# Kernel optimization log

Hardware: AMD Instinct MI355X
Metric: run time of the kernel (lower is better)

The kernel has to match this reference:

```python
import jax, jax.numpy as jnp
import numpy as np

D_MODEL = 2048
N_HEADS = 16
D_HEAD = D_MODEL // N_HEADS
D_FF = 8192
EPS = 1e-6
ROPE_BASE = 10000.0


def rmsnorm(x, g):
    return x * jax.lax.rsqrt(jnp.mean(x * x, axis=-1, keepdims=True) + EPS) * g


def rotate_half(x):
    x1, x2 = jnp.split(x, 2, axis=-1)
    return jnp.concatenate((-x2, x1), axis=-1)


def rope_tables(T):
    inv_freq = 1.0 / (ROPE_BASE ** (jnp.arange(0, D_HEAD, 2, dtype=jnp.float32) / D_HEAD))
    freqs = jnp.arange(T, dtype=jnp.float32)[:, None] * inv_freq[None, :]  # [T, D_HEAD//2]
    emb = jnp.concatenate((freqs, freqs), axis=-1)  # [T, D_HEAD]
    return jnp.cos(emb), jnp.sin(emb)


def setup_inputs() -> dict:
    key = jax.random.key(0)
    ks = jax.random.split(key, 6)
    std = 0.02
    x = jax.random.normal(ks[0], (2, 2048, D_MODEL), dtype=jnp.float32)
    # weights stored (in, out) so forward is x @ W
    w_qkv = jax.random.normal(ks[1], (D_MODEL, 3 * D_MODEL), dtype=jnp.float32) * std
    w_out = jax.random.normal(ks[2], (D_MODEL, D_MODEL), dtype=jnp.float32) * std
    w_g = jax.random.normal(ks[3], (D_MODEL, D_FF), dtype=jnp.float32) * std
    w_u = jax.random.normal(ks[4], (D_MODEL, D_FF), dtype=jnp.float32) * std
    w_o = jax.random.normal(ks[5], (D_FF, D_MODEL), dtype=jnp.float32) * std
    g1 = jnp.ones((D_MODEL,), dtype=jnp.float32)
    g2 = jnp.ones((D_MODEL,), dtype=jnp.float32)
    return {"x": x, "w_qkv": w_qkv, "w_out": w_out, "g1": g1, "g2": g2,
            "w_g": w_g, "w_u": w_u, "w_o": w_o}


def reference(x, w_qkv, w_out, g1, g2, w_g, w_u, w_o):
    B, T, D = x.shape
    H, dh = N_HEADS, D_HEAD
    scale = dh ** -0.5

    h = rmsnorm(x, g1)
    qkv = h @ w_qkv  # [B, T, 3D]
    q, k, v = jnp.split(qkv, 3, axis=-1)
    # [B, H, T, dh]
    q = q.reshape(B, T, H, dh).transpose(0, 2, 1, 3)
    k = k.reshape(B, T, H, dh).transpose(0, 2, 1, 3)
    v = v.reshape(B, T, H, dh).transpose(0, 2, 1, 3)

    cos, sin = rope_tables(T)  # [T, dh] each
    cos = cos[None, None]
    sin = sin[None, None]
    q = q * cos + rotate_half(q) * sin
    k = k * cos + rotate_half(k) * sin

    scores = jnp.einsum('bhqd,bhkd->bhqk', q, k) * scale
    causal = jnp.arange(T)[None, :] <= jnp.arange(T)[:, None]  # [T, T]
    scores = jnp.where(causal[None, None], scores, -jnp.inf)
    attn = jax.nn.softmax(scores, axis=-1)
    ctx = jnp.einsum('bhqk,bhkd->bhqd', attn, v)  # [B, H, T, dh]
    ctx = ctx.transpose(0, 2, 1, 3).reshape(B, T, D)
    x = x + ctx @ w_out

    h = rmsnorm(x, g2)
    x = x + (jax.nn.silu(h @ w_g) * (h @ w_u)) @ w_o
    return x
```

## Files before the change

### kernel.cpp

```cpp
#include <hip/hip_runtime.h>

typedef __bf16 bf16x8 __attribute__((ext_vector_type(8)));
typedef float f32x4 __attribute__((ext_vector_type(4)));
typedef unsigned short u16x8 __attribute__((ext_vector_type(8)));

#define B_SZ 2
#define T_SEQ 2048
#define D_MODEL 2048
#define N_HEADS 16
#define D_HEAD 128
#define D_FF 8192
#define BT (B_SZ * T_SEQ)
#define NT (T_SEQ / 64)

__device__ __forceinline__ unsigned short f2bf(float f) {
  unsigned int u = __builtin_bit_cast(unsigned int, f);
  u += 0x7FFFu + ((u >> 16) & 1u);
  return (unsigned short)(u >> 16);
}
__device__ __forceinline__ float bf2f(unsigned short h) {
  unsigned int u = ((unsigned int)h) << 16;
  return __builtin_bit_cast(float, u);
}

__device__ __forceinline__ void load_lds16(const void* g, void* l) {
  __builtin_amdgcn_global_load_lds(
      (const __attribute__((address_space(1))) unsigned int*)g,
      (__attribute__((address_space(3))) unsigned int*)l, 16, 0, 0);
}

template <int N>
__device__ __forceinline__ void vm_gate() {
  if constexpr (N <= 0)
    asm volatile("s_waitcnt vmcnt(0)" ::: "memory");
  else if constexpr (N == 2)
    asm volatile("s_waitcnt vmcnt(2)" ::: "memory");
  else if constexpr (N == 3)
    asm volatile("s_waitcnt vmcnt(3)" ::: "memory");
  else if constexpr (N == 4)
    asm volatile("s_waitcnt vmcnt(4)" ::: "memory");
  else if constexpr (N == 6)
    asm volatile("s_waitcnt vmcnt(6)" ::: "memory");
  else
    asm volatile("s_waitcnt vmcnt(8)" ::: "memory");
}

__global__ __launch_bounds__(256) void transpose_cast_kernel(
    const float* __restrict__ in, unsigned short* __restrict__ out, int R, int C) {
  __shared__ float tile[64][65];
  const int tx = threadIdx.x, ty = threadIdx.y;
  const int c0 = blockIdx.x * 64, r0 = blockIdx.y * 64;
#pragma unroll
  for (int i = 0; i < 4; ++i) {
    const float4 v = *(const float4*)(in + (long)(r0 + ty + 16 * i) * C + c0 + tx * 4);
    float* tr = &tile[ty + 16 * i][tx * 4];
    tr[0] = v.x; tr[1] = v.y; tr[2] = v.z; tr[3] = v.w;
  }
  __syncthreads();
#pragma unroll
  for (int i = 0; i < 4; ++i) {
    const int cc = ty + 16 * i;
    ushort4 o;
    o.x = f2bf(tile[tx * 4 + 0][cc]);
    o.y = f2bf(tile[tx * 4 + 1][cc]);
    o.z = f2bf(tile[tx * 4 + 2][cc]);
    o.w = f2bf(tile[tx * 4 + 3][cc]);
    *(ushort4*)(out + (long)(c0 + cc) * R + r0 + tx * 4) = o;
  }
}

__global__ __launch_bounds__(256) void rmsnorm_cast_kernel(
    const float* __restrict__ x, const float* __restrict__ gw,
    unsigned short* __restrict__ out) {
  const int row = blockIdx.x;
  const int tid = threadIdx.x;
  const float* xr = x + (long)row * D_MODEL;
  float4 a = *(const float4*)(xr + tid * 8);
  float4 b = *(const float4*)(xr + tid * 8 + 4);
  float ss = a.x * a.x + a.y * a.y + a.z * a.z + a.w * a.w +
             b.x * b.x + b.y * b.y + b.z * b.z + b.w * b.w;
#pragma unroll
  for (int d = 1; d < 64; d <<= 1) ss += __shfl_xor(ss, d);
  __shared__ float part[4];
  if ((tid & 63) == 0) part[tid >> 6] = ss;
  __syncthreads();
  ss = part[0] + part[1] + part[2] + part[3];
  const float rs = rsqrtf(ss * (1.0f / D_MODEL) + 1e-6f);
  float4 g0 = *(const float4*)(gw + tid * 8);
  float4 g1 = *(const float4*)(gw + tid * 8 + 4);
  ushort4 o0, o1;
  o0.x = f2bf(a.x * rs * g0.x); o0.y = f2bf(a.y * rs * g0.y);
  o0.z = f2bf(a.z * rs * g0.z); o0.w = f2bf(a.w * rs * g0.w);
  o1.x = f2bf(b.x * rs * g1.x); o1.y = f2bf(b.y * rs * g1.y);
  o1.z = f2bf(b.z * rs * g1.z); o1.w = f2bf(b.w * rs * g1.w);
  unsigned short* op = out + (long)row * D_MODEL + tid * 8;
  *(ushort4*)op = o0;
  *(ushort4*)(op + 4) = o1;
}

template <int EPI, int WM, int WN, int FM, int FN, bool DUALA = false>
__global__ __launch_bounds__(WM * WN * 64, 2) void gemm_ks_kernel(
    const unsigned short* __restrict__ A, const unsigned short* __restrict__ Bt,
    void* __restrict__ Cout, const void* __restrict__ aux,
    const unsigned short* __restrict__ A2,
    int M, int N, int K, int lda, int ldb, int ldc, int cm, int cn) {
  constexpr int THREADS = WM * WN * 64;
  constexpr int BM = WM * FM * 16;
  constexpr int BN = WN * FN * 16;
  constexpr int ASLOT = BM * 32;
  constexpr int BSLOT = BN * 32;
  constexpr int RPR = THREADS / 4;
  constexpr int LPS = BM / RPR + BN / RPR;
  __shared__ unsigned short As[4 * ASLOT];
  __shared__ unsigned short Bs[4 * BSLOT];

  const int tid = threadIdx.x;
  const int lane = tid & 63, g = lane >> 4, c = lane & 15;
  const int w = tid >> 6, wr = w / WN, wc = w % WN;

  const int nbn = N / BN;
  const int bid = (int)blockIdx.x;
  const int xcd = bid & 7, idx = bid >> 3;
  const int chn = nbn / cn;
  const int crow = xcd / chn, ccol = xcd % chn;
  const int mr = idx / cn, nc2 = idx % cn;
  const int m0 = (crow * cm + mr) * BM;
  const int n0 = (ccol * cn + nc2) * BN;

  const int nks = K >> 5;
  const int srow = tid >> 2;
  const int kq8 = (tid & 3) * 8;
  const unsigned short* A_ = A + (long)m0 * lda;
  const unsigned short* A2_ = DUALA ? (A2 + (long)m0 * lda) : nullptr;
  const unsigned short* B_ = Bt + (long)n0 * ldb;

  auto stage = [&](int s) {
    const int slot = s & 3;
    const long k32 = (long)s * 32;
    const unsigned short* Ab;
    long akofs;
    if constexpr (DUALA) {
      const int khalf = K >> 1;
      const bool lo = k32 < khalf;
      Ab = lo ? A_ : A2_;
      akofs = (lo ? k32 : k32 - khalf) + kq8;
    } else {
      Ab = A_;
      akofs = k32 + kq8;
    }
    const long bkofs = k32 + kq8;
#pragma unroll
    for (int j = 0; j < BM / RPR; ++j)
      load_lds16(Ab + (long)(j * RPR + srow) * lda + akofs,
                 &As[slot * ASLOT + (j * THREADS + tid) * 8]);
#pragma unroll
    for (int j = 0; j < BN / RPR; ++j)
      load_lds16(B_ + (long)(j * RPR + srow) * ldb + bkofs,
                 &Bs[slot * BSLOT + (j * THREADS + tid) * 8]);
  };

  f32x4 acc[FM][FN] = {};

  stage(0);
  if (nks > 1) stage(1);
  if (nks > 2) stage(2);
  vm_gate<2 * LPS>();
  __builtin_amdgcn_sched_barrier(0);
  __builtin_amdgcn_s_barrier();

  for (int s = 0; s < nks; ++s) {
    const int slot = s & 3;
    const unsigned short* Ap = &As[slot * ASLOT] + (wr * FM * 16 + c) * 32 + g * 8;
    const unsigned short* Bp = &Bs[slot * BSLOT] + (wc * FN * 16 + c) * 32 + g * 8;
    bf16x8 fa[FM], fb[FN];
#pragma unroll
    for (int fm = 0; fm < FM; ++fm) fa[fm] = *(const bf16x8*)(Ap + fm * 512);
#pragma unroll
    for (int fn = 0; fn < FN; ++fn) fb[fn] = *(const bf16x8*)(Bp + fn * 512);
    if (s + 3 < nks) stage(s + 3);
    __builtin_amdgcn_s_setprio(1);
#pragma unroll
    for (int fm = 0; fm < FM; ++fm)
#pragma unroll
      for (int fn = 0; fn < FN; ++fn)
        acc[fm][fn] = __builtin_amdgcn_mfma_f32_16x16x32_bf16(fa[fm], fb[fn], acc[fm][fn], 0, 0, 0);
    __builtin_amdgcn_s_setprio(0);
    if (s + 1 == nks) break;
    if (s <= nks - 4)
      vm_gate<2 * LPS>();
    else if (s == nks - 3)
      vm_gate<LPS>();
    else
      vm_gate<0>();
    __builtin_amdgcn_sched_barrier(0);
    __builtin_amdgcn_s_barrier();
  }

#pragma unroll
  for (int fm = 0; fm < FM; ++fm) {
#pragma unroll
    for (int r = 0; r < 4; ++r) {
      const int row = m0 + wr * FM * 16 + fm * 16 + 4 * g + r;
#pragma unroll
      for (int fn = 0; fn < FN; ++fn) {
        const int col = n0 + wc * FN * 16 + fn * 16 + c;
        const long idx2 = (long)row * ldc + col;
        float v = acc[fm][fn][r];
        if constexpr (EPI == 0) {
          ((unsigned short*)Cout)[idx2] = f2bf(v);
        } else if constexpr (EPI == 1) {
          ((float*)Cout)[idx2] = v + ((const float*)aux)[idx2];
        } else {
          const float u = bf2f(((const unsigned short*)aux)[idx2]);
          const float sg = v / (1.0f + __expf(-v));
          ((unsigned short*)Cout)[idx2] = f2bf(sg * u);
        }
      }
    }
  }
}

__global__ void rope_tables_kernel(float* __restrict__ cost, float* __restrict__ sint) {
  const int idx = blockIdx.x * 256 + threadIdx.x;
  const int t = idx >> 6, i = idx & 63;
  const float invf = powf(10000.0f, -(float)i * (1.0f / 64.0f));
  const float ang = (float)t * invf;
  cost[idx] = cosf(ang);
  sint[idx] = sinf(ang);
}

__global__ __launch_bounds__(256) void rope_apply_kernel(
    unsigned short* __restrict__ qkv, const float* __restrict__ cost,
    const float* __restrict__ sint) {
  const long idx = (long)blockIdx.x * 256 + threadIdx.x;
  const int u = (int)(idx & 7);
  const int h = (int)((idx >> 3) & 15);
  const int qk = (int)((idx >> 7) & 1);
  const long row = idx >> 8;
  const int t = (int)(row & (T_SEQ - 1));
  unsigned short* p = qkv + row * (3 * D_MODEL) + qk * D_MODEL + h * D_HEAD + u * 8;
  u16x8 lo = *(const u16x8*)p;
  u16x8 hi = *(const u16x8*)(p + 64);
  const float4 c0 = *(const float4*)(cost + t * 64 + u * 8);
  const float4 c1 = *(const float4*)(cost + t * 64 + u * 8 + 4);
  const float4 s0 = *(const float4*)(sint + t * 64 + u * 8);
  const float4 s1 = *(const float4*)(sint + t * 64 + u * 8 + 4);
  const float cv[8] = {c0.x, c0.y, c0.z, c0.w, c1.x, c1.y, c1.z, c1.w};
  const float sv[8] = {s0.x, s0.y, s0.z, s0.w, s1.x, s1.y, s1.z, s1.w};
  u16x8 ro, rh;
#pragma unroll
  for (int j = 0; j < 8; ++j) {
    const float a = bf2f(lo[j]);
    const float b = bf2f(hi[j]);
    ro[j] = f2bf(a * cv[j] - b * sv[j]);
    rh[j] = f2bf(b * cv[j] + a * sv[j]);
  }
  *(u16x8*)p = ro;
  *(u16x8*)(p + 64) = rh;
}

__global__ __launch_bounds__(256) void vtrans_kernel(
    const unsigned short* __restrict__ qkv, unsigned short* __restrict__ vt) {
  __shared__ unsigned short tile[64][68];
  const int tx = threadIdx.x, ty = threadIdx.y;
  const int t0 = blockIdx.x * 64, d0 = blockIdx.y * 64;
  const int bh = blockIdx.z;
  const int b = bh >> 4, h = bh & 15;
#pragma unroll
  for (int i = 0; i < 4; ++i) {
    const ushort4 v = *(const ushort4*)(
        qkv + (long)(b * T_SEQ + t0 + ty + 16 * i) * (3 * D_MODEL) + 2 * D_MODEL +
        h * D_HEAD + d0 + tx * 4);
    unsigned short* tr = &tile[ty + 16 * i][tx * 4];
    tr[0] = v.x; tr[1] = v.y; tr[2] = v.z; tr[3] = v.w;
  }
  __syncthreads();
#pragma unroll
  for (int i = 0; i < 4; ++i) {
    const int dd = ty + 16 * i;
    ushort4 o;
    o.x = tile[tx * 4 + 0][dd];
    o.y = tile[tx * 4 + 1][dd];
    o.z = tile[tx * 4 + 2][dd];
    o.w = tile[tx * 4 + 3][dd];
    *(ushort4*)(vt + ((long)bh * D_HEAD + d0 + dd) * T_SEQ + t0 + tx * 4) = o;
  }
}

__global__ __launch_bounds__(256) void attn_kernel(
    const unsigned short* __restrict__ qkv, const unsigned short* __restrict__ vt,
    unsigned short* __restrict__ ctx) {
  __shared__ unsigned short Ks[2][64 * 128];
  __shared__ unsigned short Vs[2][128 * 64];
  const int h = blockIdx.y, b = blockIdx.z;
  const int tid = threadIdx.x;
  const int w = tid >> 6, lane = tid & 63, g = lane >> 4, c = lane & 15;
  const float scale = 0.08838834764831845f;
  const int srcA = (2 * (g & 1)) * 16 + c;
  const int srcB = srcA + 16;
  const bool hi = (g >> 1) != 0;
  const int bh = b * N_HEADS + h;

  const int ssk = (tid & 15) ^ ((tid >> 4) & 7);
  const int ssv = (tid & 7) ^ ((tid >> 3) & 7);
  const unsigned short* Kg = qkv + (long)b * T_SEQ * 3 * D_MODEL + D_MODEL + (long)h * D_HEAD;
  const unsigned short* Vg = vt + (long)bh * D_HEAD * T_SEQ;

  auto stage = [&](int kv0, int bufi) {
#pragma unroll
    for (int i = 0; i < 4; ++i) {
      const int rowk = i * 16 + (tid >> 4);
      load_lds16(Kg + (long)(kv0 + rowk) * (3 * D_MODEL) + ssk * 8,
                 &Ks[bufi][(i * 256 + tid) * 8]);
    }
#pragma unroll
    for (int i = 0; i < 4; ++i) {
      const int rowv = i * 32 + (tid >> 3);
      load_lds16(Vg + (long)rowv * T_SEQ + kv0 + ssv * 8,
                 &Vs[bufi][(i * 256 + tid) * 8]);
    }
  };

  const int cs7 = c & 7;

  for (int pass = 0; pass < 2; ++pass) {
    const int qt = pass ? (NT - 1 - blockIdx.x) : blockIdx.x;
    const int q = qt * 64 + w * 16 + c;

    bf16x8 fq[4];
    const long rowQ = (long)(b * T_SEQ + q) * (3 * D_MODEL) + h * D_HEAD;
#pragma unroll
    for (int ks = 0; ks < 4; ++ks)
      fq[ks] = *(const bf16x8*)(qkv + rowQ + ks * 32 + g * 8);

    f32x4 o[8] = {};
    float mrun = -INFINITY, ell = 0.0f;

    stage(0, 0);
    asm volatile("s_waitcnt vmcnt(0)" ::: "memory");
    __syncthreads();
    int buf = 0;

    for (int kt = 0; kt <= qt; ++kt) {
      const int kv0 = kt * 64;
      if (kt < qt) stage(kv0 + 64, buf ^ 1);

      f32x4 s[4] = {};
      __builtin_amdgcn_s_setprio(1);
#pragma unroll
      for (int fm = 0; fm < 4; ++fm) {
        const unsigned short* kr = &Ks[buf][(fm * 16 + c) * 128];
#pragma unroll
        for (int ks = 0; ks < 4; ++ks) {
          bf16x8 ak = *(const bf16x8*)(kr + ((ks * 4 + g) ^ cs7) * 8);
          s[fm] = __builtin_amdgcn_mfma_f32_16x16x32_bf16(ak, fq[ks], s[fm], 0, 0, 0);
        }
      }
      __builtin_amdgcn_s_setprio(0);
      float pmax = -INFINITY;
      const bool diag = (kt == qt);
#pragma unroll
      for (int fm = 0; fm < 4; ++fm)
#pragma unroll
        for (int r = 0; r < 4; ++r) {
          float sv = s[fm][r] * scale;
          if (diag) {
            const int kp = kv0 + fm * 16 + 4 * g + r;
            if (kp > q) sv = -INFINITY;
          }
          s[fm][r] = sv;
          pmax = fmaxf(pmax, sv);
        }
      pmax = fmaxf(pmax, __shfl_xor(pmax, 16));
      pmax = fmaxf(pmax, __shfl_xor(pmax, 32));
      const float mnew = fmaxf(mrun, pmax);
      const float resc = __expf(mrun - mnew);
      mrun = mnew;
      float rowsum = 0.0f;
#pragma unroll
      for (int fm = 0; fm < 4; ++fm)
#pragma unroll
        for (int r = 0; r < 4; ++r) {
          const float p = __expf(s[fm][r] - mnew);
          s[fm][r] = p;
          rowsum += p;
        }
      rowsum += __shfl_xor(rowsum, 16);
      rowsum += __shfl_xor(rowsum, 32);
      ell = ell * resc + rowsum;
#pragma unroll
      for (int fm = 0; fm < 8; ++fm) o[fm] *= resc;

      bf16x8 pb[2];
#pragma unroll
      for (int k2 = 0; k2 < 2; ++k2) {
        float va[4], vb[4];
#pragma unroll
        for (int r = 0; r < 4; ++r) {
          const float t0 = __shfl(s[k2 * 2][r], srcA);
          const float t1 = __shfl(s[k2 * 2 + 1][r], srcA);
          va[r] = hi ? t1 : t0;
          const float u0 = __shfl(s[k2 * 2][r], srcB);
          const float u1 = __shfl(s[k2 * 2 + 1][r], srcB);
          vb[r] = hi ? u1 : u0;
        }
        bf16x8 pv;
        pv[0] = (__bf16)va[0]; pv[1] = (__bf16)va[1];
        pv[2] = (__bf16)va[2]; pv[3] = (__bf16)va[3];
        pv[4] = (__bf16)vb[0]; pv[5] = (__bf16)vb[1];
        pv[6] = (__bf16)vb[2]; pv[7] = (__bf16)vb[3];
        pb[k2] = pv;
      }
      __builtin_amdgcn_s_setprio(1);
#pragma unroll
      for (int fm = 0; fm < 8; ++fm) {
        const unsigned short* vr = &Vs[buf][(fm * 16 + c) * 64];
#pragma unroll
        for (int k2 = 0; k2 < 2; ++k2) {
          bf16x8 av = *(const bf16x8*)(vr + ((k2 * 4 + g) ^ cs7) * 8);
          o[fm] = __builtin_amdgcn_mfma_f32_16x16x32_bf16(av, pb[k2], o[fm], 0, 0, 0);
        }
      }
      __builtin_amdgcn_s_setprio(0);
      asm volatile("s_waitcnt vmcnt(0)" ::: "memory");
      __syncthreads();
      buf ^= 1;
    }

    const float inv = 1.0f / ell;
    unsigned short* outp = ctx + (long)(b * T_SEQ + q) * D_MODEL + h * D_HEAD;
#pragma unroll
    for (int fm = 0; fm < 8; ++fm) {
      ushort4 pk;
      pk.x = f2bf(o[fm][0] * inv);
      pk.y = f2bf(o[fm][1] * inv);
      pk.z = f2bf(o[fm][2] * inv);
      pk.w = f2bf(o[fm][3] * inv);
      *(ushort4*)(outp + fm * 16 + 4 * g) = pk;
    }
  }
}

extern "C" void kernel_launch(void* const* d_in, const int* in_sizes, int n_in,
                              void* d_out, int out_size, void* d_ws, size_t ws_size,
                              hipStream_t stream) {
  const float* x = (const float*)d_in[0];
  const float* w_qkv = (const float*)d_in[1];
  const float* w_out = (const float*)d_in[2];
  const float* g1 = (const float*)d_in[3];
  const float* g2 = (const float*)d_in[4];
  const float* w_g = (const float*)d_in[5];
  const float* w_u = (const float*)d_in[6];
  const float* w_o = (const float*)d_in[7];
  float* out = (float*)d_out;

  char* ws = (char*)d_ws;
  size_t off = 0;
  auto take = [&](size_t bytes) {
    char* p = ws + off;
    off += (bytes + 255) & ~(size_t)255;
    return p;
  };

  char* Wreg = take((size_t)3 * D_FF * D_MODEL * 2);
  unsigned short* wTqkv = (unsigned short*)Wreg;
  unsigned short* wTout = (unsigned short*)(Wreg + (size_t)3 * D_MODEL * D_MODEL * 2);
  unsigned short* wTg = (unsigned short*)Wreg;
  unsigned short* wTu = (unsigned short*)(Wreg + (size_t)D_FF * D_MODEL * 2);
  unsigned short* wTo = (unsigned short*)(Wreg + (size_t)2 * D_FF * D_MODEL * 2);

  const size_t qkv_b = (size_t)BT * 3 * D_MODEL * 2;
  const size_t vt_b = (size_t)B_SZ * N_HEADS * D_HEAD * T_SEQ * 2;
  const size_t ctx_b = (size_t)BT * D_MODEL * 2;
  char* AR = take(qkv_b + vt_b + ctx_b);
  unsigned short* qkvb = (unsigned short*)AR;
  unsigned short* vtb = (unsigned short*)(AR + qkv_b);
  unsigned short* ctxb = (unsigned short*)(AR + qkv_b + vt_b);
  unsigned short* gbuf0 = (unsigned short*)AR;
  unsigned short* gbuf1 = (unsigned short*)(AR + (size_t)BT * (D_FF / 2) * 2);

  float* x1 = (float*)take((size_t)BT * D_MODEL * 4);
  unsigned short* hb = (unsigned short*)take((size_t)BT * D_MODEL * 2);
  float* cost = (float*)take((size_t)T_SEQ * 64 * 4);
  float* sint = (float*)take((size_t)T_SEQ * 64 * 4);

  const dim3 tb(16, 16);

  transpose_cast_kernel<<<dim3(3 * D_MODEL / 64, D_MODEL / 64), tb, 0, stream>>>(w_qkv, wTqkv, D_MODEL, 3 * D_MODEL);
  transpose_cast_kernel<<<dim3(D_MODEL / 64, D_MODEL / 64), tb, 0, stream>>>(w_out, wTout, D_MODEL, D_MODEL);
  rope_tables_kernel<<<T_SEQ * 64 / 256, 256, 0, stream>>>(cost, sint);

  rmsnorm_cast_kernel<<<BT, 256, 0, stream>>>(x, g1, hb);
  gemm_ks_kernel<0, 2, 4, 8, 4><<<384, 512, 0, stream>>>(
      hb, wTqkv, qkvb, nullptr, nullptr, BT, 3 * D_MODEL, D_MODEL, D_MODEL, D_MODEL, 3 * D_MODEL, 8, 6);
  rope_apply_kernel<<<(BT * N_HEADS * 2 * 8) / 256, 256, 0, stream>>>(qkvb, cost, sint);
  vtrans_kernel<<<dim3(T_SEQ / 64, D_HEAD / 64, B_SZ * N_HEADS), tb, 0, stream>>>(qkvb, vtb);
  attn_kernel<<<dim3(NT / 2, N_HEADS, B_SZ), 256, 0, stream>>>(qkvb, vtb, ctxb);
  gemm_ks_kernel<1, 4, 2, 4, 4><<<256, 512, 0, stream>>>(
      ctxb, wTout, x1, x, nullptr, BT, D_MODEL, D_MODEL, D_MODEL, D_MODEL, D_MODEL, 8, 4);

  transpose_cast_kernel<<<dim3(D_FF / 64, D_MODEL / 64), tb, 0, stream>>>(w_g, wTg, D_MODEL, D_FF);
  transpose_cast_kernel<<<dim3(D_FF / 64, D_MODEL / 64), tb, 0, stream>>>(w_u, wTu, D_MODEL, D_FF);
  transpose_cast_kernel<<<dim3(D_MODEL / 64, D_FF / 64), tb, 0, stream>>>(w_o, wTo, D_FF, D_MODEL);
  rmsnorm_cast_kernel<<<BT, 256, 0, stream>>>(x1, g2, hb);

  const int NH = D_FF / 2;
  for (int half = 0; half < 2; ++half) {
    const unsigned short* wTu_h = wTu + (size_t)half * NH * D_MODEL;
    const unsigned short* wTg_h = wTg + (size_t)half * NH * D_MODEL;
    unsigned short* gb = half ? gbuf1 : gbuf0;
    gemm_ks_kernel<0, 2, 4, 8, 4><<<256, 512, 0, stream>>>(
        hb, wTu_h, gb, nullptr, nullptr, BT, NH, D_MODEL, D_MODEL, D_MODEL, NH, 4, 8);
    gemm_ks_kernel<2, 2, 4, 8, 4><<<256, 512, 0, stream>>>(
        hb, wTg_h, gb, gb, nullptr, BT, NH, D_MODEL, D_MODEL, D_MODEL, NH, 4, 8);
  }
  gemm_ks_kernel<1, 4, 2, 4, 4, true><<<256, 512, 0, stream>>>(
      gbuf0, wTo, out, x1, gbuf1, BT, D_MODEL, D_FF, NH, D_FF, D_MODEL, 8, 4);
}
```

Before: 778.8 us.

## Fuse gate and up projections into one dual-accumulator GEMM with SiLU epilogue

Replaces the separate up-projection GEMM and the gate GEMM (which re-read the up result from memory) with a single kernel. It streams the shared A tile once and keeps two accumulator sets for the gate and up weights, applying SiLU*up in the epilogue. This removes the bf16 write and read of the intermediate up buffer and halves the A-tile loads. In exchange it doubles accumulator registers (launch bounds 512,1) and uses a larger LDS footprint with a 3-stage pipeline, which may limit occupancy.

```diff
diff --git a/kernel.cpp b/kernel.cpp
--- a/kernel.cpp
+++ b/kernel.cpp
@@ -39,8 +39,12 @@
     asm volatile("s_waitcnt vmcnt(3)" ::: "memory");
   else if constexpr (N == 4)
     asm volatile("s_waitcnt vmcnt(4)" ::: "memory");
+  else if constexpr (N == 5)
+    asm volatile("s_waitcnt vmcnt(5)" ::: "memory");
   else if constexpr (N == 6)
     asm volatile("s_waitcnt vmcnt(6)" ::: "memory");
+  else if constexpr (N == 10)
+    asm volatile("s_waitcnt vmcnt(10)" ::: "memory");
   else
     asm volatile("s_waitcnt vmcnt(8)" ::: "memory");
 }
@@ -215,6 +219,108 @@
           const float sg = v / (1.0f + __expf(-v));
           ((unsigned short*)Cout)[idx2] = f2bf(sg * u);
         }
+      }
+    }
+  }
+}
+
+__global__ __launch_bounds__(512, 1) void gemm_gu_kernel(
+    const unsigned short* __restrict__ A, const unsigned short* __restrict__ Bg,
+    const unsigned short* __restrict__ Bu, unsigned short* __restrict__ Cout,
+    int M, int N, int K, int lda, int ldb, int ldc, int cm, int cn) {
+  constexpr int BM = 128, BN = 256;
+  constexpr int ASLOT = BM * 32;
+  constexpr int BSLOT = BN * 32;
+  __shared__ unsigned short As[3 * ASLOT];
+  __shared__ unsigned short Bgs[3 * BSLOT];
+  __shared__ unsigned short Bus[3 * BSLOT];
+
+  const int tid = threadIdx.x;
+  const int lane = tid & 63, g = lane >> 4, c = lane & 15;
+  const int w = tid >> 6, wr = w >> 2, wc = w & 3;
+
+  const int nbn = N / BN;
+  const int bid = (int)blockIdx.x;
+  const int xcd = bid & 7, idx = bid >> 3;
+  const int chn = nbn / cn;
+  const int crow = xcd / chn, ccol = xcd % chn;
+  const int m0 = (crow * cm + idx / cn) * BM;
+  const int n0 = (ccol * cn + idx % cn) * BN;
+
+  const int nks = K >> 5;
+  const int srow = tid >> 2;
+  const int kq8 = (tid & 3) * 8;
+  const unsigned short* A_ = A + (long)m0 * lda;
+  const unsigned short* Bg_ = Bg + (long)n0 * ldb;
+  const unsigned short* Bu_ = Bu + (long)n0 * ldb;
+
+  auto stage = [&](int s) {
+    const int slot = s % 3;
+    const long kofs = (long)s * 32 + kq8;
+    load_lds16(A_ + (long)srow * lda + kofs, &As[slot * ASLOT + tid * 8]);
+#pragma unroll
+    for (int j = 0; j < 2; ++j)
+      load_lds16(Bg_ + (long)(j * 128 + srow) * ldb + kofs,
+                 &Bgs[slot * BSLOT + (j * 512 + tid) * 8]);
+#pragma unroll
+    for (int j = 0; j < 2; ++j)
+      load_lds16(Bu_ + (long)(j * 128 + srow) * ldb + kofs,
+                 &Bus[slot * BSLOT + (j * 512 + tid) * 8]);
+  };
+
+  f32x4 accG[4][4] = {};
+  f32x4 accU[4][4] = {};
+
+  stage(0);
+  if (nks > 1) stage(1);
+  vm_gate<5>();
+  __builtin_amdgcn_sched_barrier(0);
+  __builtin_amdgcn_s_barrier();
+
+  for (int s = 0; s < nks; ++s) {
+    const int slot = s % 3;
+    const unsigned short* Ap = &As[slot * ASLOT] + (wr * 64 + c) * 32 + g * 8;
+    const unsigned short* Bgp = &Bgs[slot * BSLOT] + (wc * 64 + c) * 32 + g * 8;
+    const unsigned short* Bup = &Bus[slot * BSLOT] + (wc * 64 + c) * 32 + g * 8;
+    bf16x8 fa[4], fbg[4], fbu[4];
+#pragma unroll
+    for (int fm = 0; fm < 4; ++fm) fa[fm] = *(const bf16x8*)(Ap + fm * 512);
+#pragma unroll
+    for (int fn = 0; fn < 4; ++fn) {
+      fbg[fn] = *(const bf16x8*)(Bgp + fn * 512);
+      fbu[fn] = *(const bf16x8*)(Bup + fn * 512);
+    }
+    if (s + 2 < nks) stage(s + 2);
+    __builtin_amdgcn_s_setprio(1);
+#pragma unroll
+    for (int fm = 0; fm < 4; ++fm)
+#pragma unroll
+      for (int fn = 0; fn < 4; ++fn) {
+        accG[fm][fn] = __builtin_amdgcn_mfma_f32_16x16x32_bf16(fa[fm], fbg[fn], accG[fm][fn], 0, 0, 0);
+        accU[fm][fn] = __builtin_amdgcn_mfma_f32_16x16x32_bf16(fa[fm], fbu[fn], accU[fm][fn], 0, 0, 0);
+      }
+    __builtin_amdgcn_s_setprio(0);
+    if (s + 1 == nks) break;
+    if (s + 2 < nks)
+      vm_gate<5>();
+    else
+      vm_gate<0>();
+    __builtin_amdgcn_sched_barrier(0);
+    __builtin_amdgcn_s_barrier();
+  }
+
+#pragma unroll
+  for (int fm = 0; fm < 4; ++fm) {
+#pragma unroll
+    for (int r = 0; r < 4; ++r) {
+      const int row = m0 + wr * 64 + fm * 16 + 4 * g + r;
+#pragma unroll
+      for (int fn = 0; fn < 4; ++fn) {
+        const int col = n0 + wc * 64 + fn * 16 + c;
+        const float gv = accG[fm][fn][r];
+        const float uv = accU[fm][fn][r];
+        const float sg = gv / (1.0f + __expf(-gv));
+        Cout[(long)row * ldc + col] = f2bf(sg * uv);
       }
     }
   }
@@ -509,10 +615,8 @@
     const unsigned short* wTu_h = wTu + (size_t)half * NH * D_MODEL;
     const unsigned short* wTg_h = wTg + (size_t)half * NH * D_MODEL;
     unsigned short* gb = half ? gbuf1 : gbuf0;
-    gemm_ks_kernel<0, 2, 4, 8, 4><<<256, 512, 0, stream>>>(
-        hb, wTu_h, gb, nullptr, nullptr, BT, NH, D_MODEL, D_MODEL, D_MODEL, NH, 4, 8);
-    gemm_ks_kernel<2, 2, 4, 8, 4><<<256, 512, 0, stream>>>(
-        hb, wTg_h, gb, gb, nullptr, BT, NH, D_MODEL, D_MODEL, D_MODEL, NH, 4, 8);
+    gemm_gu_kernel<<<512, 512, 0, stream>>>(
+        hb, wTg_h, wTu_h, gb, BT, NH, D_MODEL, D_MODEL, D_MODEL, NH, 8, 8);
   }
   gemm_ks_kernel<1, 4, 2, 4, 4, true><<<256, 512, 0, stream>>>(
       gbuf0, wTo, out, x1, gbuf1, BT, D_MODEL, D_FF, NH, D_FF, D_MODEL, 8, 4);
```

Measured after the change: 779.8 us. About the same (+0.1%).
